# Kernel optimization log

Measured on AMD Instinct MI355X. Metric: run time of the kernel, lower is better.

Reference implementation:

```python
import jax, jax.numpy as jnp
import numpy as np

B, S, D_MODEL, D_K = 4, 4096, 1024, 128
NEG = jnp.float32(-1e30)  # acts as -inf for masking; exp underflows to exactly 0 in fp32


def setup_inputs() -> dict:
    key = jax.random.key(0)
    ks = jax.random.split(key, 8)
    sc = 1.0 / np.sqrt(D_MODEL)
    x = jax.random.normal(ks[0], (B, S, D_MODEL), jnp.float32)
    padding_mask = (jax.random.uniform(ks[1], (B, S)) > 0.05).astype(jnp.float32)
    Wq = jax.random.normal(ks[2], (D_MODEL, D_K), jnp.float32) * sc
    bq = jax.random.normal(ks[3], (D_K,), jnp.float32) * 0.01
    Wk = jax.random.normal(ks[4], (D_MODEL, D_K), jnp.float32) * sc
    bk = jax.random.normal(ks[5], (D_K,), jnp.float32) * 0.01
    Wv = jax.random.normal(ks[6], (D_MODEL, D_K), jnp.float32) * sc
    bv = jax.random.normal(ks[7], (D_K,), jnp.float32) * 0.01
    return {"x": x, "padding_mask": padding_mask, "Wq": Wq, "bq": bq,
            "Wk": Wk, "bk": bk, "Wv": Wv, "bv": bv}


def reference(x, padding_mask, Wq, bq, Wk, bk, Wv, bv):
    # Self-attention path (enc_dec_layer_input is None), masked=True (causal).
    scale = jnp.sqrt(jnp.float32(Wq.shape[-1]))
    Q = x @ Wq + bq  # [B,S,Dk]
    K = x @ Wk + bk
    V = x @ Wv + bv
    scores = jnp.einsum('bqd,bkd->bqk', Q, K) / scale  # [B,S,S]
    # causal mask (torch: triu(1) filled with -inf) AND padding outer-product mask
    causal = jnp.tril(jnp.ones((S, S), dtype=bool))  # True = allowed
    pm = (padding_mask[:, :, None] * padding_mask[:, None, :]) > 0  # [B,S,S]
    allowed = causal[None] & pm
    scores = jnp.where(allowed, scores, NEG)
    attn = jax.nn.softmax(scores, axis=-1)
    # torch: fully-masked query rows give NaN -> nan_to_num -> 0.
    # A query row is dead iff its own token is padded (diagonal is causally allowed).
    row_alive = padding_mask > 0  # [B,S]
    attn = jnp.where(row_alive[:, :, None], attn, 0.0)
    out = jnp.einsum('bqk,bkd->bqd', attn, V)  # [B,S,Dk]
    return out
```

## Files before the change

### kernel.cpp

```cpp
#include <hip/hip_runtime.h>
#include <hip/hip_bf16.h>
#include <cstdint>

typedef __bf16 bf16x8 __attribute__((ext_vector_type(8)));
typedef float f32x4 __attribute__((ext_vector_type(4)));

#define MFMA16(a, b, c) __builtin_amdgcn_mfma_f32_16x16x32_bf16((a), (b), (c), 0, 0, 0)

__device__ __forceinline__ unsigned short f2bf(float f) {
  union { float f; unsigned u; } v; v.f = f;
  unsigned u = v.u;
  u += 0x7fffu + ((u >> 16) & 1u);
  return (unsigned short)(u >> 16);
}
__device__ __forceinline__ unsigned pk2(float a, float b) {
  __hip_bfloat162 h = __float22bfloat162_rn(make_float2(a, b));
  union { __hip_bfloat162 h; unsigned u; } v; v.h = h; return v.u;
}

__global__ __launch_bounds__(256) void convert_w(
    const float* __restrict__ Wq, const float* __restrict__ Wk,
    const float* __restrict__ Wv, unsigned short* __restrict__ wt) {
  int idx = blockIdx.x * 256 + threadIdx.x;
  int m = idx >> 17;
  int rem = idx & 131071;
  int k = rem >> 7;
  int n = rem & 127;
  const float* W = (m == 0) ? Wq : (m == 1) ? Wk : Wv;
  wt[(size_t)m * 131072 + (size_t)n * 1024 + k] = f2bf(W[(size_t)k * 128 + n]);
}

__global__ __launch_bounds__(256) void qkv_gemm(
    const float* __restrict__ x, const unsigned short* __restrict__ wt_all,
    const float* __restrict__ bq, const float* __restrict__ bk,
    const float* __restrict__ bv,
    unsigned short* __restrict__ Qg, unsigned short* __restrict__ Kg,
    unsigned short* __restrict__ Vtg) {
  __shared__ unsigned short x_lds[128][40];
  __shared__ unsigned short w_lds[128][40];
  const int tid = threadIdx.x;
  const int lane = tid & 63;
  const int w = tid >> 6;
  const int mode = blockIdx.y;
  const int m0 = blockIdx.x * 128;
  const unsigned short* wt = wt_all + (size_t)mode * 131072;
  const float* bias = (mode == 0) ? bq : (mode == 1) ? bk : bv;

  const int wr = (w >> 1) * 64;
  const int wc = (w & 1) * 64;
  const int lr = lane & 15;
  const int lk = (lane >> 4) * 8;

  f32x4 acc[4][4];
#pragma unroll
  for (int m = 0; m < 4; ++m)
#pragma unroll
    for (int n = 0; n < 4; ++n) acc[m][n] = (f32x4){0.f, 0.f, 0.f, 0.f};

  const int srow = tid >> 1;
  const int shalf = (tid & 1) * 16;
  const float* xrow = x + (size_t)(m0 + srow) * 1024 + shalf;
  const unsigned short* wrow = wt + (size_t)srow * 1024 + shalf;

  float4 xa, xb, xc, xd; uint4 wv0, wv1;
  {
    const float4* s4 = (const float4*)xrow;
    xa = s4[0]; xb = s4[1]; xc = s4[2]; xd = s4[3];
    const uint4* ws4 = (const uint4*)wrow;
    wv0 = ws4[0]; wv1 = ws4[1];
  }

  for (int k0 = 0; k0 < 1024; k0 += 32) {
    __syncthreads();
    {
      uint4 w0, w1;
      w0.x = pk2(xa.x, xa.y);  w0.y = pk2(xa.z, xa.w);
      w0.z = pk2(xb.x, xb.y);  w0.w = pk2(xb.z, xb.w);
      w1.x = pk2(xc.x, xc.y);  w1.y = pk2(xc.z, xc.w);
      w1.z = pk2(xd.x, xd.y);  w1.w = pk2(xd.z, xd.w);
      *(uint4*)&x_lds[srow][shalf] = w0;
      *(uint4*)&x_lds[srow][shalf + 8] = w1;
      *(uint4*)&w_lds[srow][shalf] = wv0;
      *(uint4*)&w_lds[srow][shalf + 8] = wv1;
    }
    __syncthreads();
    if (k0 + 32 < 1024) {
      const float4* s4 = (const float4*)(xrow + k0 + 32);
      xa = s4[0]; xb = s4[1]; xc = s4[2]; xd = s4[3];
      const uint4* ws4 = (const uint4*)(wrow + k0 + 32);
      wv0 = ws4[0]; wv1 = ws4[1];
    }
    bf16x8 af[4], bfr[4];
#pragma unroll
    for (int m = 0; m < 4; ++m) af[m] = *(const bf16x8*)&x_lds[wr + m * 16 + lr][lk];
#pragma unroll
    for (int n = 0; n < 4; ++n) bfr[n] = *(const bf16x8*)&w_lds[wc + n * 16 + lr][lk];
#pragma unroll
    for (int m = 0; m < 4; ++m)
#pragma unroll
      for (int n = 0; n < 4; ++n) acc[m][n] = MFMA16(af[m], bfr[n], acc[m][n]);
  }

  float bcol[4];
#pragma unroll
  for (int n = 0; n < 4; ++n) bcol[n] = bias[wc + n * 16 + lr];
#pragma unroll
  for (int m = 0; m < 4; ++m)
#pragma unroll
    for (int n = 0; n < 4; ++n)
#pragma unroll
      for (int r = 0; r < 4; ++r) {
        int grow = m0 + wr + m * 16 + (lane >> 4) * 4 + r;
        int col = wc + n * 16 + lr;
        float val = acc[m][n][r] + bcol[n];
        if (mode == 0) {
          val *= 0.08838834764831845f;
          Qg[(size_t)grow * 128 + col] = f2bf(val);
        } else if (mode == 1) {
          Kg[(size_t)grow * 128 + col] = f2bf(val);
        } else {
          int bb = grow >> 12, s = grow & 4095;
          Vtg[((size_t)bb * 128 + col) * 4096 + s] = f2bf(val);
        }
      }
}

struct AttnLds {
  unsigned short K_lds[64][136];
  unsigned short V_lds[128][72];
  unsigned short P_lds[4][16][68];
};

__device__ __forceinline__ void attn_tiles(
    AttnLds& S, const unsigned short* __restrict__ Kg,
    const unsigned short* __restrict__ Vtg, const float* __restrict__ pmask,
    int b, int q0, int tstart, int tend,
    const bf16x8 (&qf)[4], float& mrow, float& lsum, f32x4 (&o)[8]) {
  const int tid = threadIdx.x;
  const int lane = tid & 63;
  const int w = tid >> 6;
  const int lr = lane & 15;
  const int lg = lane >> 4;
  const int lk = lg * 8;
  const int q_own = q0 + w * 16 + lr;

  for (int t = tstart; t < tend; ++t) {
    const int k0 = t * 64;
    __syncthreads();
    {
      int kr = tid >> 2, seg = (tid & 3) * 32;
      const uint4* src = (const uint4*)(Kg + ((size_t)b * 4096 + k0 + kr) * 128 + seg);
      uint4 v0 = src[0], v1 = src[1], v2 = src[2], v3 = src[3];
      uint4* dst = (uint4*)&S.K_lds[kr][seg];
      dst[0] = v0; dst[1] = v1; dst[2] = v2; dst[3] = v3;
      int d = tid >> 1, half = (tid & 1) * 32;
      const uint4* vs = (const uint4*)(Vtg + ((size_t)b * 128 + d) * 4096 + k0 + half);
      uint4 u0 = vs[0], u1 = vs[1], u2 = vs[2], u3 = vs[3];
      uint4* vdst = (uint4*)&S.V_lds[d][half];
      vdst[0] = u0; vdst[1] = u1; vdst[2] = u2; vdst[3] = u3;
    }
    __syncthreads();

    f32x4 st[4];
#pragma unroll
    for (int f = 0; f < 4; ++f) {
      st[f] = (f32x4){0.f, 0.f, 0.f, 0.f};
#pragma unroll
      for (int dc = 0; dc < 4; ++dc) {
        bf16x8 kf = *(const bf16x8*)&S.K_lds[f * 16 + lr][dc * 32 + lk];
        st[f] = MFMA16(kf, qf[dc], st[f]);
      }
    }

    const unsigned long long mb = __ballot(pmask[(size_t)b * 4096 + k0 + lane] > 0.f);
    unsigned nib[4];
#pragma unroll
    for (int f = 0; f < 4; ++f) nib[f] = (unsigned)(mb >> (16 * f + 4 * lg)) & 0xFu;

    float mx = -1e30f;
    if (k0 + 63 > q0 + (w << 4)) {
#pragma unroll
      for (int f = 0; f < 4; ++f)
#pragma unroll
        for (int r = 0; r < 4; ++r) {
          const bool ok = (((nib[f] >> r) & 1u) != 0u) &&
                          (k0 + 16 * f + 4 * lg + r <= q_own);
          const float s = ok ? st[f][r] : -1e30f;
          st[f][r] = s;
          mx = fmaxf(mx, s);
        }
    } else {
#pragma unroll
      for (int f = 0; f < 4; ++f)
#pragma unroll
        for (int r = 0; r < 4; ++r) {
          const bool ok = ((nib[f] >> r) & 1u) != 0u;
          const float s = ok ? st[f][r] : -1e30f;
          st[f][r] = s;
          mx = fmaxf(mx, s);
        }
    }
    mx = fmaxf(mx, __shfl_xor(mx, 16));
    mx = fmaxf(mx, __shfl_xor(mx, 32));
    const float mnew = fmaxf(mrow, mx);
    const float alpha = __expf(mrow - mnew);
    mrow = mnew;

    float sum = 0.f;
#pragma unroll
    for (int f = 0; f < 4; ++f) {
      const float p0 = (st[f][0] < -1e29f) ? 0.f : __expf(st[f][0] - mnew);
      const float p1 = (st[f][1] < -1e29f) ? 0.f : __expf(st[f][1] - mnew);
      const float p2 = (st[f][2] < -1e29f) ? 0.f : __expf(st[f][2] - mnew);
      const float p3 = (st[f][3] < -1e29f) ? 0.f : __expf(st[f][3] - mnew);
      sum += (p0 + p1) + (p2 + p3);
      uint2 u; u.x = pk2(p0, p1); u.y = pk2(p2, p3);
      *(uint2*)&S.P_lds[w][lr][16 * f + 4 * lg] = u;
    }
    sum += __shfl_xor(sum, 16);
    sum += __shfl_xor(sum, 32);
    lsum = lsum * alpha + sum;
#pragma unroll
    for (int n = 0; n < 8; ++n) o[n] *= alpha;

    __asm__ volatile("s_waitcnt lgkmcnt(0)" ::: "memory");
#pragma unroll
    for (int kc = 0; kc < 2; ++kc) {
      bf16x8 pa = *(const bf16x8*)&S.P_lds[w][lr][kc * 32 + lk];
#pragma unroll
      for (int n = 0; n < 8; ++n) {
        bf16x8 vf = *(const bf16x8*)&S.V_lds[n * 16 + lr][kc * 32 + lk];
        o[n] = MFMA16(vf, pa, o[n]);
      }
    }
  }
}

__global__ __launch_bounds__(256) void attn_fwd(
    const unsigned short* __restrict__ Qg, const unsigned short* __restrict__ Kg,
    const unsigned short* __restrict__ Vtg, const float* __restrict__ pmask,
    float* __restrict__ out) {
  __shared__ AttnLds S;
  const int tid = threadIdx.x;
  const int lane = tid & 63;
  const int w = tid >> 6;
  const int b = blockIdx.y;
  const int q0 = blockIdx.x * 64;
  const int lr = lane & 15;
  const int lg = lane >> 4;
  const int lk = lg * 8;

  bf16x8 qf[4];
  {
    const unsigned short* qp = Qg + ((size_t)b * 4096 + q0 + w * 16 + lr) * 128;
#pragma unroll
    for (int dc = 0; dc < 4; ++dc) qf[dc] = *(const bf16x8*)(qp + dc * 32 + lk);
  }
  float mrow = -1e30f, lsum = 0.f;
  f32x4 o[8];
#pragma unroll
  for (int n = 0; n < 8; ++n) o[n] = (f32x4){0.f, 0.f, 0.f, 0.f};

  attn_tiles(S, Kg, Vtg, pmask, b, q0, 0, (q0 >> 6) + 1, qf, mrow, lsum, o);

  const int qrow = q0 + w * 16 + lr;
  const bool alive = pmask[(size_t)b * 4096 + qrow] > 0.f;
  const float inv = (alive && lsum > 0.f) ? 1.f / lsum : 0.f;
  float* op = out + ((size_t)b * 4096 + qrow) * 128 + 4 * lg;
#pragma unroll
  for (int n = 0; n < 8; ++n) {
    f32x4 v = o[n] * inv;
    *(f32x4*)(op + n * 16) = v;
  }
}

__global__ __launch_bounds__(256) void attn_split(
    const unsigned short* __restrict__ Qg, const unsigned short* __restrict__ Kg,
    const unsigned short* __restrict__ Vtg, const float* __restrict__ pmask,
    float* __restrict__ out, float* __restrict__ o_part,
    float* __restrict__ ml_part) {
  __shared__ AttnLds S;
  const int tid = threadIdx.x;
  const int lane = tid & 63;
  const int w = tid >> 6;
  const int L = blockIdx.x;
  const int xcd = L & 7;
  const int b = xcd >> 1;
  const int s = ((L >> 3) << 1) | (xcd & 1);
  int qb, c, nch;
  if (s < 16)      { qb = s;                c = 0;          nch = 1; }
  else if (s < 48) { int t = s - 16; qb = 16 + (t >> 1); c = t & 1;  nch = 2; }
  else if (s < 96) { int t = s - 48; qb = 32 + t / 3;    c = t % 3;  nch = 3; }
  else             { int t = s - 96; qb = 48 + (t >> 2); c = t & 3;  nch = 4; }
  const int q0 = qb * 64;
  const int tstart = c * 16;
  const int tend = min(c * 16 + 16, qb + 1);
  const int lr = lane & 15;
  const int lg = lane >> 4;
  const int lk = lg * 8;

  bf16x8 qf[4];
  {
    const unsigned short* qp = Qg + ((size_t)b * 4096 + q0 + w * 16 + lr) * 128;
#pragma unroll
    for (int dc = 0; dc < 4; ++dc) qf[dc] = *(const bf16x8*)(qp + dc * 32 + lk);
  }
  float mrow = -1e30f, lsum = 0.f;
  f32x4 o[8];
#pragma unroll
  for (int n = 0; n < 8; ++n) o[n] = (f32x4){0.f, 0.f, 0.f, 0.f};

  attn_tiles(S, Kg, Vtg, pmask, b, q0, tstart, tend, qf, mrow, lsum, o);

  if (nch == 1) {
    const int qrow = q0 + w * 16 + lr;
    const bool alive = pmask[(size_t)b * 4096 + qrow] > 0.f;
    const float inv = (alive && lsum > 0.f) ? 1.f / lsum : 0.f;
    float* op = out + ((size_t)b * 4096 + qrow) * 128 + 4 * lg;
#pragma unroll
    for (int n = 0; n < 8; ++n) {
      f32x4 v = o[n] * inv;
      *(f32x4*)(op + n * 16) = v;
    }
  } else {
    const int slot = (b * 64 + qb) * 4 + c;
    float* op = o_part + ((size_t)slot * 64 + w * 16 + lr) * 128 + 4 * lg;
#pragma unroll
    for (int n = 0; n < 8; ++n) *(f32x4*)(op + n * 16) = o[n];
    if (lane < 16) {
      float* mp = ml_part + ((size_t)slot * 64 + w * 16 + lane) * 2;
      mp[0] = mrow;
      mp[1] = lsum;
    }
  }
}

__global__ __launch_bounds__(256) void attn_combine(
    const float* __restrict__ o_part, const float* __restrict__ ml_part,
    const float* __restrict__ pmask, float* __restrict__ out) {
  const int tid = threadIdx.x;
  const int lane = tid & 63;
  const int w = tid >> 6;
  const int g = blockIdx.x * 4 + w;
  const int b = g / 3072;
  const int rem = g % 3072;
  const int qb = 16 + (rem >> 6);
  const int row = rem & 63;
  const int qrow = qb * 64 + row;
  const int nch = (qb >> 4) + 1;
  const int pbase = (b * 64 + qb) * 4;

  float m[4], l[4];
  float M = -1e30f;
  for (int c = 0; c < nch; ++c) {
    const float* mp = ml_part + ((size_t)(pbase + c) * 64 + row) * 2;
    m[c] = mp[0];
    l[c] = mp[1];
    M = fmaxf(M, m[c]);
  }
  float L = 0.f, wgt[4];
  for (int c = 0; c < nch; ++c) {
    wgt[c] = __expf(m[c] - M);
    L += wgt[c] * l[c];
  }
  float2 acc = {0.f, 0.f};
  for (int c = 0; c < nch; ++c) {
    const float2 v = *(const float2*)(o_part + ((size_t)(pbase + c) * 64 + row) * 128 + lane * 2);
    acc.x += wgt[c] * v.x;
    acc.y += wgt[c] * v.y;
  }
  const bool alive = pmask[(size_t)b * 4096 + qrow] > 0.f;
  const float inv = (alive && L > 0.f) ? 1.f / L : 0.f;
  float2* op = (float2*)(out + ((size_t)b * 4096 + qrow) * 128);
  op[lane] = make_float2(acc.x * inv, acc.y * inv);
}

extern "C" void kernel_launch(void* const* d_in, const int* in_sizes, int n_in,
                              void* d_out, int out_size, void* d_ws, size_t ws_size,
                              hipStream_t stream) {
  (void)in_sizes; (void)n_in; (void)out_size;
  const float* x  = (const float*)d_in[0];
  const float* pm = (const float*)d_in[1];
  const float* Wq = (const float*)d_in[2];
  const float* bq = (const float*)d_in[3];
  const float* Wk = (const float*)d_in[4];
  const float* bk = (const float*)d_in[5];
  const float* Wv = (const float*)d_in[6];
  const float* bv = (const float*)d_in[7];
  float* out = (float*)d_out;

  unsigned short* ws  = (unsigned short*)d_ws;
  unsigned short* wt  = ws;
  unsigned short* Qg  = ws + 393216;
  unsigned short* Kg  = Qg + 2097152;
  unsigned short* Vtg = Kg + 2097152;
  float* o_part  = (float*)(ws + 6684672);
  float* ml_part = o_part + 8388608;
  const size_t WS_NEED = 13369344u + (8388608u + 131072u) * 4u;

  convert_w<<<1536, 256, 0, stream>>>(Wq, Wk, Wv, wt);
  qkv_gemm<<<dim3(128, 3), 256, 0, stream>>>(x, wt, bq, bk, bv, Qg, Kg, Vtg);
  if (ws_size >= WS_NEED) {
    attn_split<<<640, 256, 0, stream>>>(Qg, Kg, Vtg, pm, out, o_part, ml_part);
    attn_combine<<<3072, 256, 0, stream>>>(o_part, ml_part, pm, out);
  } else {
    attn_fwd<<<dim3(64, 4), 256, 0, stream>>>(Qg, Kg, Vtg, pm, out);
  }
}
```

Measured before the change: 123.7 us.

## Double-buffer K/V tiles with direct global-to-LDS loads and XOR swizzle

K and V tiles now go straight from global memory into LDS with global_load_lds, into two alternating buffers, so the next tile is prefetched while the current one is consumed. This drops the second barrier per iteration and the round trip through registers. Padded LDS rows are replaced by an XOR swizzle on 16-byte chunks to avoid bank conflicts, and s_setprio raises wave priority around the MFMA blocks. It doubles K/V LDS usage, which can lower occupancy. Correctness depends on the compiler waiting for the async LDS loads to finish before the barrier.

```diff
diff --git a/kernel.cpp b/kernel.cpp
--- a/kernel.cpp
+++ b/kernel.cpp
@@ -6,6 +6,10 @@
 typedef float f32x4 __attribute__((ext_vector_type(4)));
 
 #define MFMA16(a, b, c) __builtin_amdgcn_mfma_f32_16x16x32_bf16((a), (b), (c), 0, 0, 0)
+
+#define GLL16(g, l) __builtin_amdgcn_global_load_lds( \
+    (const __attribute__((address_space(1))) unsigned int*)(g), \
+    (__attribute__((address_space(3))) unsigned int*)(l), 16, 0, 0)
 
 __device__ __forceinline__ unsigned short f2bf(float f) {
   union { float f; unsigned u; } v; v.f = f;
@@ -126,10 +130,33 @@
 }
 
 struct AttnLds {
-  unsigned short K_lds[64][136];
-  unsigned short V_lds[128][72];
+  unsigned short K_lds[2][64][128];
+  unsigned short V_lds[2][128][64];
   unsigned short P_lds[4][16][68];
 };
+
+__device__ __forceinline__ void stage_kv(AttnLds& S, int buf,
+    const unsigned short* __restrict__ Kb, const unsigned short* __restrict__ Vb,
+    int k0, int w, int lane) {
+#pragma unroll
+  for (int j = 0; j < 4; ++j) {
+    const int cid = j * 4 + w;
+    {
+      const int s = cid * 64 + lane;
+      const int row = s >> 4, cp = s & 15;
+      const int csrc = cp ^ (row & 7);
+      GLL16(Kb + (size_t)(k0 + row) * 128 + csrc * 8,
+            &S.K_lds[buf][0][0] + cid * 512);
+    }
+    {
+      const int s = cid * 64 + lane;
+      const int row = s >> 3, cp = s & 7;
+      const int csrc = cp ^ (row & 7);
+      GLL16(Vb + (size_t)row * 4096 + k0 + csrc * 8,
+            &S.V_lds[buf][0][0] + cid * 512);
+    }
+  }
+}
 
 __device__ __forceinline__ void attn_tiles(
     AttnLds& S, const unsigned short* __restrict__ Kg,
@@ -141,36 +168,31 @@
   const int w = tid >> 6;
   const int lr = lane & 15;
   const int lg = lane >> 4;
-  const int lk = lg * 8;
+  const int sw = lr & 7;
   const int q_own = q0 + w * 16 + lr;
+  const unsigned short* Kb = Kg + (size_t)b * 4096 * 128;
+  const unsigned short* Vb = Vtg + (size_t)b * 128 * 4096;
+
+  int buf = 0;
+  stage_kv(S, 0, Kb, Vb, tstart * 64, w, lane);
 
   for (int t = tstart; t < tend; ++t) {
     const int k0 = t * 64;
     __syncthreads();
-    {
-      int kr = tid >> 2, seg = (tid & 3) * 32;
-      const uint4* src = (const uint4*)(Kg + ((size_t)b * 4096 + k0 + kr) * 128 + seg);
-      uint4 v0 = src[0], v1 = src[1], v2 = src[2], v3 = src[3];
-      uint4* dst = (uint4*)&S.K_lds[kr][seg];
-      dst[0] = v0; dst[1] = v1; dst[2] = v2; dst[3] = v3;
-      int d = tid >> 1, half = (tid & 1) * 32;
-      const uint4* vs = (const uint4*)(Vtg + ((size_t)b * 128 + d) * 4096 + k0 + half);
-      uint4 u0 = vs[0], u1 = vs[1], u2 = vs[2], u3 = vs[3];
-      uint4* vdst = (uint4*)&S.V_lds[d][half];
-      vdst[0] = u0; vdst[1] = u1; vdst[2] = u2; vdst[3] = u3;
-    }
-    __syncthreads();
+    if (t + 1 < tend) stage_kv(S, buf ^ 1, Kb, Vb, (t + 1) * 64, w, lane);
 
     f32x4 st[4];
+    __builtin_amdgcn_s_setprio(1);
 #pragma unroll
     for (int f = 0; f < 4; ++f) {
       st[f] = (f32x4){0.f, 0.f, 0.f, 0.f};
 #pragma unroll
       for (int dc = 0; dc < 4; ++dc) {
-        bf16x8 kf = *(const bf16x8*)&S.K_lds[f * 16 + lr][dc * 32 + lk];
+        bf16x8 kf = *(const bf16x8*)&S.K_lds[buf][f * 16 + lr][(((dc << 2) | lg) ^ sw) << 3];
         st[f] = MFMA16(kf, qf[dc], st[f]);
       }
     }
+    __builtin_amdgcn_s_setprio(0);
 
     const unsigned long long mb = __ballot(pmask[(size_t)b * 4096 + k0 + lane] > 0.f);
     unsigned nib[4];
@@ -224,15 +246,18 @@
     for (int n = 0; n < 8; ++n) o[n] *= alpha;
 
     __asm__ volatile("s_waitcnt lgkmcnt(0)" ::: "memory");
+    __builtin_amdgcn_s_setprio(1);
 #pragma unroll
     for (int kc = 0; kc < 2; ++kc) {
-      bf16x8 pa = *(const bf16x8*)&S.P_lds[w][lr][kc * 32 + lk];
+      bf16x8 pa = *(const bf16x8*)&S.P_lds[w][lr][kc * 32 + lg * 8];
 #pragma unroll
       for (int n = 0; n < 8; ++n) {
-        bf16x8 vf = *(const bf16x8*)&S.V_lds[n * 16 + lr][kc * 32 + lk];
+        bf16x8 vf = *(const bf16x8*)&S.V_lds[buf][n * 16 + lr][(((kc << 2) | lg) ^ sw) << 3];
         o[n] = MFMA16(vf, pa, o[n]);
       }
     }
+    __builtin_amdgcn_s_setprio(0);
+    buf ^= 1;
   }
 }
 
```

After: 132.5 us. +7.1%, slower.
